# Optimization experiments

Measured on AMD Instinct MI355X. Metric: run time of the kernel, lower is better.

Reference implementation:

```python
import jax, jax.numpy as jnp
import numpy as np

N_SRC = 100_000
N_NODES = 1_000_000
N_NEIGH = 20
RAW_DIM = 256
NEIGH_DIM = 128
MSG_DIM = 128


def setup_inputs() -> dict:
    key = jax.random.key(0)
    ks = jax.random.split(key, 8)
    s = 0.05
    return {
        "raw_messages": jax.random.normal(ks[0], (N_SRC, RAW_DIM), dtype=jnp.float32),
        "neighbors": jax.random.randint(ks[1], (N_SRC, N_NEIGH), 0, N_NODES, dtype=jnp.int64),
        "memory": jax.random.normal(ks[2], (N_NODES, NEIGH_DIM), dtype=jnp.float32),
        "W1": jax.random.normal(ks[3], (RAW_DIM, RAW_DIM // 2), dtype=jnp.float32) * s,
        "b1": jnp.zeros((RAW_DIM // 2,), dtype=jnp.float32),
        "W2": jax.random.normal(ks[4], (RAW_DIM // 2, MSG_DIM), dtype=jnp.float32) * s,
        "b2": jnp.zeros((MSG_DIM,), dtype=jnp.float32),
        "Wn": jax.random.normal(ks[5], (NEIGH_DIM, MSG_DIM), dtype=jnp.float32) * s,
        "bn": jnp.zeros((MSG_DIM,), dtype=jnp.float32),
    }


def reference(raw_messages, neighbors, memory, W1, b1, W2, b2, Wn, bn):
    # Gather neighbor memories: [N, K, D_neigh]
    neighbor_memories = memory[neighbors]
    # Mean-pool over the K sampled neighbors: [N, D_neigh]
    neighbor_agg = neighbor_memories.mean(axis=1)
    # message_sum MLP: Linear -> ReLU -> Linear -> ReLU
    h = jax.nn.relu(raw_messages @ W1 + b1)
    a = jax.nn.relu(h @ W2 + b2)
    # neighbor_sum MLP: Linear -> ReLU
    b = jax.nn.relu(neighbor_agg @ Wn + bn)
    return a + b
```

## Files before the change

### kernel.cpp

```cpp
#include <hip/hip_runtime.h>

#define N_SRC    100000
#define N_NODES  1000000
#define N_NEIGH  20
#define DRAW     256
#define DH       128
#define DMSG     128
#define DNEI     128
#define LDS_PAD  8

typedef __bf16 bf16x8 __attribute__((ext_vector_type(8)));
typedef float  floatx4 __attribute__((ext_vector_type(4)));
typedef unsigned int uint32;

#define OFF_W1T   (0ull)
#define OFF_W2T   (64ull * 1024)
#define OFF_WNT   (96ull * 1024)
#define OFF_H     (1ull << 20)
#define OFF_AGG   (32ull << 20)
#define OFF_MEMBF (64ull << 20)
#define WS_NEED   (320ull << 20)

#define G1_BLOCKS   1563
#define K2_PERIODS  521
#define K2_TOTAL    (K2_PERIODS * 7)
#define CV_BLOCKS   (K2_PERIODS * 4)
#define NCHUNK      ((size_t)N_NODES * DNEI / 8)

__global__ void convert_weights(const float* __restrict__ W1,
                                const float* __restrict__ W2,
                                const float* __restrict__ Wn,
                                __bf16* __restrict__ W1t,
                                __bf16* __restrict__ W2t,
                                __bf16* __restrict__ Wnt) {
    int i = blockIdx.x * 256 + threadIdx.x;
    if (i < 32768) {
        int n = i >> 8, k = i & 255;
        W1t[i] = (__bf16)W1[k * 128 + n];
    } else if (i < 49152) {
        int j = i - 32768;
        int n = j >> 7, k = j & 127;
        W2t[j] = (__bf16)W2[k * 128 + n];
    } else {
        int j = i - 49152;
        int n = j >> 7, k = j & 127;
        Wnt[j] = (__bf16)Wn[k * 128 + n];
    }
}

__global__ __launch_bounds__(256)
void convert_and_gemm1(const float* __restrict__ raw,
                       const float* __restrict__ memv,
                       const float* __restrict__ b1,
                       const __bf16* __restrict__ W1t,
                       __bf16* __restrict__ membf,
                       __bf16* __restrict__ h) {
    __shared__ __bf16 hbuf[64][DH + LDS_PAD];

    const int bid = blockIdx.x;
    const int tid = threadIdx.x;
    const int r   = bid % 7;
    const int p   = bid / 7;

    if (r >= 3) {
        const int cvid = p * 4 + (r - 3);
        size_t c = (size_t)cvid * 256 + tid;
        const size_t stride = (size_t)CV_BLOCKS * 256;
        for (; c < NCHUNK; c += stride) {
            const floatx4* src = reinterpret_cast<const floatx4*>(memv + c * 8);
            floatx4 a = __builtin_nontemporal_load(src);
            floatx4 b = __builtin_nontemporal_load(src + 1);
            bf16x8 o;
            o[0]=(__bf16)a[0]; o[1]=(__bf16)a[1]; o[2]=(__bf16)a[2]; o[3]=(__bf16)a[3];
            o[4]=(__bf16)b[0]; o[5]=(__bf16)b[1]; o[6]=(__bf16)b[2]; o[7]=(__bf16)b[3];
            *reinterpret_cast<bf16x8*>(membf + c * 8) = o;
        }
        return;
    }

    const int g1id = p * 3 + r;
    const int s0   = g1id * 64;
    const int lane = tid & 63;
    const int wave = tid >> 6;
    const int mr   = lane & 15;
    const int quad = lane >> 4;

    {
        int rowg = s0 + wave * 16 + mr;
        int rowc = rowg < N_SRC ? rowg : N_SRC - 1;
        const float* ar = raw + (size_t)rowc * DRAW;

        floatx4 acc[8];
        #pragma unroll
        for (int nt = 0; nt < 8; ++nt) { floatx4 z = {0.f,0.f,0.f,0.f}; acc[nt] = z; }

        #pragma unroll
        for (int kk = 0; kk < DRAW; kk += 32) {
            const int kb = kk + quad * 8;
            floatx4 a0 = __builtin_nontemporal_load(
                reinterpret_cast<const floatx4*>(ar + kb));
            floatx4 a1 = __builtin_nontemporal_load(
                reinterpret_cast<const floatx4*>(ar + kb) + 1);
            bf16x8 af;
            af[0]=(__bf16)a0[0]; af[1]=(__bf16)a0[1]; af[2]=(__bf16)a0[2]; af[3]=(__bf16)a0[3];
            af[4]=(__bf16)a1[0]; af[5]=(__bf16)a1[1]; af[6]=(__bf16)a1[2]; af[7]=(__bf16)a1[3];
            #pragma unroll
            for (int nt = 0; nt < 8; ++nt) {
                bf16x8 bf = *reinterpret_cast<const bf16x8*>(
                    W1t + (nt * 16 + mr) * DRAW + kb);
                acc[nt] = __builtin_amdgcn_mfma_f32_16x16x32_bf16(af, bf, acc[nt], 0, 0, 0);
            }
        }
        #pragma unroll
        for (int nt = 0; nt < 8; ++nt) {
            const int col  = nt * 16 + mr;
            const float bias = b1[col];
            #pragma unroll
            for (int rr = 0; rr < 4; ++rr) {
                int mrow = wave * 16 + quad * 4 + rr;
                float v = acc[nt][rr] + bias;
                hbuf[mrow][col] = (__bf16)(v > 0.f ? v : 0.f);
            }
        }
    }

    __syncthreads();

    const int cr = tid >> 4;
    const int cc = (tid & 15) * 8;
    #pragma unroll
    for (int it = 0; it < 4; ++it) {
        int row = cr + it * 16;
        int rg  = s0 + row;
        if (rg < N_SRC) {
            *reinterpret_cast<bf16x8*>(h + (size_t)rg * DH + cc) =
                *reinterpret_cast<const bf16x8*>(&hbuf[row][cc]);
        }
    }
}

__global__ __launch_bounds__(256)
void gather_bf16(const int*    __restrict__ neigh,
                 const __bf16* __restrict__ membf,
                 __bf16*       __restrict__ aggb) {
    int wid0 = blockIdx.x * 4 + (threadIdx.x >> 6);
    const int wid  = __builtin_amdgcn_readfirstlane(wid0);
    const int lane = threadIdx.x & 63;
    if (wid >= N_SRC) return;

    const int* nb = neigh + wid * N_NEIGH;
    uint32 v[N_NEIGH];
    #pragma unroll
    for (int n = 0; n < N_NEIGH; ++n) {
        int idx = nb[n];
        v[n] = *reinterpret_cast<const uint32*>(
            membf + (size_t)idx * DNEI + lane * 2);
    }
    float sx = 0.f, sy = 0.f;
    #pragma unroll
    for (int n = 0; n < N_NEIGH; ++n) {
        sx += __builtin_bit_cast(float, v[n] << 16);
        sy += __builtin_bit_cast(float, v[n] & 0xffff0000u);
    }
    const float inv = 1.0f / N_NEIGH;
    __bf16 r0 = (__bf16)(sx * inv);
    __bf16 r1 = (__bf16)(sy * inv);
    union { __bf16 b[2]; uint32 u; } pk;
    pk.b[0] = r0; pk.b[1] = r1;
    *reinterpret_cast<uint32*>(aggb + (size_t)wid * DNEI + lane * 2) = pk.u;
}

__global__ __launch_bounds__(256)
void gemm23(const __bf16* __restrict__ h,
            const __bf16* __restrict__ aggb,
            const float*  __restrict__ b2,
            const float*  __restrict__ bn,
            const __bf16* __restrict__ W2t,
            const __bf16* __restrict__ Wnt,
            float* __restrict__ out) {
    const int tid  = threadIdx.x;
    const int s0   = blockIdx.x * 64;
    const int lane = tid & 63;
    const int wave = tid >> 6;
    const int mr   = lane & 15;
    const int quad = lane >> 4;

    const int rowg = s0 + wave * 16 + mr;
    const int rowc = rowg < N_SRC ? rowg : N_SRC - 1;

    bf16x8 af2[4], af3[4];
    #pragma unroll
    for (int i = 0; i < 4; ++i) {
        const int kb = i * 32 + quad * 8;
        af2[i] = *reinterpret_cast<const bf16x8*>(h    + (size_t)rowc * DH   + kb);
        af3[i] = *reinterpret_cast<const bf16x8*>(aggb + (size_t)rowc * DNEI + kb);
    }

    floatx4 acc2[8], acc3[8];
    #pragma unroll
    for (int nt = 0; nt < 8; ++nt) {
        floatx4 z = {0.f,0.f,0.f,0.f}; acc2[nt] = z; acc3[nt] = z;
    }

    #pragma unroll
    for (int i = 0; i < 4; ++i) {
        const int kb = i * 32 + quad * 8;
        #pragma unroll
        for (int nt = 0; nt < 8; ++nt) {
            bf16x8 bw2 = *reinterpret_cast<const bf16x8*>(
                W2t + (nt * 16 + mr) * DH + kb);
            acc2[nt] = __builtin_amdgcn_mfma_f32_16x16x32_bf16(af2[i], bw2, acc2[nt], 0, 0, 0);
            bf16x8 bw3 = *reinterpret_cast<const bf16x8*>(
                Wnt + (nt * 16 + mr) * DNEI + kb);
            acc3[nt] = __builtin_amdgcn_mfma_f32_16x16x32_bf16(af3[i], bw3, acc3[nt], 0, 0, 0);
        }
    }

    #pragma unroll
    for (int nt = 0; nt < 8; ++nt) {
        const int col = nt * 16 + mr;
        const float bb2 = b2[col];
        const float bbn = bn[col];
        #pragma unroll
        for (int rr = 0; rr < 4; ++rr) {
            int rowl = wave * 16 + quad * 4 + rr;
            int rg   = s0 + rowl;
            if (rg < N_SRC) {
                float va = acc2[nt][rr] + bb2; va = va > 0.f ? va : 0.f;
                float vb = acc3[nt][rr] + bbn; vb = vb > 0.f ? vb : 0.f;
                out[(size_t)rg * DMSG + col] = va + vb;
            }
        }
    }
}

__global__ __launch_bounds__(256)
void gather_mean(const int*   __restrict__ neigh,
                 const float* __restrict__ memv,
                 float*       __restrict__ agg) {
    const int wid  = blockIdx.x * 4 + (threadIdx.x >> 6);
    const int lane = threadIdx.x & 63;
    if (wid >= N_SRC) return;

    int myidx = 0;
    if (lane < N_NEIGH) myidx = neigh[wid * N_NEIGH + lane];

    float2 v[N_NEIGH];
    #pragma unroll
    for (int n = 0; n < N_NEIGH; ++n) {
        int idx = __shfl(myidx, n, 64);
        v[n] = reinterpret_cast<const float2*>(memv + (size_t)idx * DNEI)[lane];
    }
    float sx = 0.f, sy = 0.f;
    #pragma unroll
    for (int n = 0; n < N_NEIGH; ++n) { sx += v[n].x; sy += v[n].y; }
    const float inv = 1.0f / N_NEIGH;
    float2 rr; rr.x = sx * inv; rr.y = sy * inv;
    reinterpret_cast<float2*>(agg + (size_t)wid * DNEI)[lane] = rr;
}

__global__ __launch_bounds__(256)
void mlp_kernel(const float* __restrict__ raw,
                const float* __restrict__ agg,
                const float* __restrict__ b1,
                const float* __restrict__ b2,
                const float* __restrict__ bn,
                const __bf16* __restrict__ W1t,
                const __bf16* __restrict__ W2t,
                const __bf16* __restrict__ Wnt,
                float* __restrict__ out) {
    __shared__ __bf16 hbuf[64][DH + LDS_PAD];

    const int tid  = threadIdx.x;
    const int s0   = blockIdx.x * 64;
    const int lane = tid & 63;
    const int wave = tid >> 6;
    const int mr   = lane & 15;
    const int quad = lane >> 4;

    const int rowg = s0 + wave * 16 + mr;
    const int rowc = rowg < N_SRC ? rowg : N_SRC - 1;

    float4 ag[8];
    {
        const float* ar3 = agg + (size_t)rowc * DNEI;
        #pragma unroll
        for (int i = 0; i < 4; ++i) {
            ag[2 * i]     = *reinterpret_cast<const float4*>(ar3 + i * 32 + quad * 8);
            ag[2 * i + 1] = *reinterpret_cast<const float4*>(ar3 + i * 32 + quad * 8 + 4);
        }
    }

    {
        const float* ar = raw + (size_t)rowc * DRAW;
        floatx4 acc[8];
        #pragma unroll
        for (int nt = 0; nt < 8; ++nt) { floatx4 z = {0.f,0.f,0.f,0.f}; acc[nt] = z; }

        #pragma unroll
        for (int kk = 0; kk < DRAW; kk += 32) {
            const int kb = kk + quad * 8;
            float4 a0 = *reinterpret_cast<const float4*>(ar + kb);
            float4 a1 = *reinterpret_cast<const float4*>(ar + kb + 4);
            bf16x8 af;
            af[0]=(__bf16)a0.x; af[1]=(__bf16)a0.y; af[2]=(__bf16)a0.z; af[3]=(__bf16)a0.w;
            af[4]=(__bf16)a1.x; af[5]=(__bf16)a1.y; af[6]=(__bf16)a1.z; af[7]=(__bf16)a1.w;
            #pragma unroll
            for (int nt = 0; nt < 8; ++nt) {
                bf16x8 bf = *reinterpret_cast<const bf16x8*>(
                    W1t + (nt * 16 + mr) * DRAW + kb);
                acc[nt] = __builtin_amdgcn_mfma_f32_16x16x32_bf16(af, bf, acc[nt], 0, 0, 0);
            }
        }
        #pragma unroll
        for (int nt = 0; nt < 8; ++nt) {
            const int col  = nt * 16 + mr;
            const float bias = b1[col];
            #pragma unroll
            for (int rr = 0; rr < 4; ++rr) {
                int mrow = wave * 16 + quad * 4 + rr;
                float v = acc[nt][rr] + bias;
                hbuf[mrow][col] = (__bf16)(v > 0.f ? v : 0.f);
            }
        }
    }

    __syncthreads();

    {
        floatx4 acc2[8], acc3[8];
        #pragma unroll
        for (int nt = 0; nt < 8; ++nt) {
            floatx4 z = {0.f,0.f,0.f,0.f}; acc2[nt] = z; acc3[nt] = z;
        }

        #pragma unroll
        for (int kk = 0; kk < DH; kk += 32) {
            const int kb = kk + quad * 8;
            const int i  = kk >> 5;
            bf16x8 af2 = *reinterpret_cast<const bf16x8*>(&hbuf[wave * 16 + mr][kb]);
            bf16x8 af3;
            {
                float4 g0 = ag[2 * i], g1 = ag[2 * i + 1];
                af3[0]=(__bf16)g0.x; af3[1]=(__bf16)g0.y; af3[2]=(__bf16)g0.z; af3[3]=(__bf16)g0.w;
                af3[4]=(__bf16)g1.x; af3[5]=(__bf16)g1.y; af3[6]=(__bf16)g1.z; af3[7]=(__bf16)g1.w;
            }
            #pragma unroll
            for (int nt = 0; nt < 8; ++nt) {
                bf16x8 bw2 = *reinterpret_cast<const bf16x8*>(
                    W2t + (nt * 16 + mr) * DH + kb);
                acc2[nt] = __builtin_amdgcn_mfma_f32_16x16x32_bf16(af2, bw2, acc2[nt], 0, 0, 0);
                bf16x8 bw3 = *reinterpret_cast<const bf16x8*>(
                    Wnt + (nt * 16 + mr) * DNEI + kb);
                acc3[nt] = __builtin_amdgcn_mfma_f32_16x16x32_bf16(af3, bw3, acc3[nt], 0, 0, 0);
            }
        }

        #pragma unroll
        for (int nt = 0; nt < 8; ++nt) {
            const int col = nt * 16 + mr;
            const float bb2 = b2[col];
            const float bbn = bn[col];
            #pragma unroll
            for (int rr = 0; rr < 4; ++rr) {
                int rowl = wave * 16 + quad * 4 + rr;
                int rg   = s0 + rowl;
                if (rg < N_SRC) {
                    float va = acc2[nt][rr] + bb2; va = va > 0.f ? va : 0.f;
                    float vb = acc3[nt][rr] + bbn; vb = vb > 0.f ? vb : 0.f;
                    out[(size_t)rg * DMSG + col] = va + vb;
                }
            }
        }
    }
}

extern "C" void kernel_launch(void* const* d_in, const int* in_sizes, int n_in,
                              void* d_out, int out_size, void* d_ws, size_t ws_size,
                              hipStream_t stream) {
    const float* raw   = (const float*)d_in[0];
    const int*   neigh = (const int*)  d_in[1];
    const float* memv  = (const float*)d_in[2];
    const float* W1    = (const float*)d_in[3];
    const float* b1    = (const float*)d_in[4];
    const float* W2    = (const float*)d_in[5];
    const float* b2    = (const float*)d_in[6];
    const float* Wn    = (const float*)d_in[7];
    const float* bn    = (const float*)d_in[8];
    float* out = (float*)d_out;

    __bf16* W1t = (__bf16*)((char*)d_ws + OFF_W1T);
    __bf16* W2t = (__bf16*)((char*)d_ws + OFF_W2T);
    __bf16* Wnt = (__bf16*)((char*)d_ws + OFF_WNT);

    convert_weights<<<dim3(256), dim3(256), 0, stream>>>(W1, W2, Wn, W1t, W2t, Wnt);

    if (ws_size >= WS_NEED) {
        __bf16* h     = (__bf16*)((char*)d_ws + OFF_H);
        __bf16* aggb  = (__bf16*)((char*)d_ws + OFF_AGG);
        __bf16* membf = (__bf16*)((char*)d_ws + OFF_MEMBF);

        convert_and_gemm1<<<dim3(K2_TOTAL), dim3(256), 0, stream>>>(
            raw, memv, b1, W1t, membf, h);
        gather_bf16<<<dim3((N_SRC + 3) / 4), dim3(256), 0, stream>>>(
            neigh, membf, aggb);
        gemm23<<<dim3(G1_BLOCKS), dim3(256), 0, stream>>>(
            h, aggb, b2, bn, W2t, Wnt, out);
    } else {
        float* agg = out;
        gather_mean<<<dim3((N_SRC + 3) / 4), dim3(256), 0, stream>>>(neigh, memv, agg);
        mlp_kernel<<<dim3(G1_BLOCKS), dim3(256), 0, stream>>>(
            raw, agg, b1, b2, bn, W1t, W2t, Wnt, out);
    }
}
```

Before: 932.2 us.

## Split memory conversion, use 16-byte gather, fuse all three GEMMs into one kernel

Moves the fp32-to-bf16 memory conversion into its own kernel instead of interleaving it with GEMM1 blocks. The gather is rewritten so each lane loads 16 bytes and four neighbors are fetched per wave step, then reduced with cross-lane shuffles. GEMM1 is fused with GEMM2/GEMM3, keeping h in LDS so the bf16 h round-trip through global memory goes away. The cost is that the old overlap of conversion with GEMM1 is lost, and the fused kernel needs more registers.

```diff
diff --git a/kernel.cpp b/kernel.cpp
--- a/kernel.cpp
+++ b/kernel.cpp
@@ -12,20 +12,17 @@
 typedef __bf16 bf16x8 __attribute__((ext_vector_type(8)));
 typedef float  floatx4 __attribute__((ext_vector_type(4)));
 typedef unsigned int uint32;
+typedef uint32 uint32x4 __attribute__((ext_vector_type(4)));
 
 #define OFF_W1T   (0ull)
 #define OFF_W2T   (64ull * 1024)
 #define OFF_WNT   (96ull * 1024)
-#define OFF_H     (1ull << 20)
 #define OFF_AGG   (32ull << 20)
 #define OFF_MEMBF (64ull << 20)
 #define WS_NEED   (320ull << 20)
 
-#define G1_BLOCKS   1563
-#define K2_PERIODS  521
-#define K2_TOTAL    (K2_PERIODS * 7)
-#define CV_BLOCKS   (K2_PERIODS * 4)
-#define NCHUNK      ((size_t)N_NODES * DNEI / 8)
+#define G1_BLOCKS 1563
+#define NCHUNK    ((size_t)N_NODES * DNEI / 8)
 
 __global__ void convert_weights(const float* __restrict__ W1,
                                 const float* __restrict__ W2,
@@ -49,135 +46,83 @@
 }
 
 __global__ __launch_bounds__(256)
-void convert_and_gemm1(const float* __restrict__ raw,
-                       const float* __restrict__ memv,
-                       const float* __restrict__ b1,
-                       const __bf16* __restrict__ W1t,
-                       __bf16* __restrict__ membf,
-                       __bf16* __restrict__ h) {
+void convert_mem(const float* __restrict__ memv, __bf16* __restrict__ membf) {
+    size_t c = (size_t)blockIdx.x * 256 + threadIdx.x;
+    const size_t stride = (size_t)gridDim.x * 256;
+    for (; c < NCHUNK; c += stride) {
+        const floatx4* src = reinterpret_cast<const floatx4*>(memv + c * 8);
+        floatx4 a = __builtin_nontemporal_load(src);
+        floatx4 b = __builtin_nontemporal_load(src + 1);
+        bf16x8 o;
+        o[0]=(__bf16)a[0]; o[1]=(__bf16)a[1]; o[2]=(__bf16)a[2]; o[3]=(__bf16)a[3];
+        o[4]=(__bf16)b[0]; o[5]=(__bf16)b[1]; o[6]=(__bf16)b[2]; o[7]=(__bf16)b[3];
+        *reinterpret_cast<bf16x8*>(membf + c * 8) = o;
+    }
+}
+
+__global__ __launch_bounds__(256)
+void gather4(const int*    __restrict__ neigh,
+             const __bf16* __restrict__ membf,
+             __bf16*       __restrict__ aggb) {
+    const int tid   = threadIdx.x;
+    const int lane  = tid & 63;
+    const int wave  = tid >> 6;
+    const int slot  = lane >> 4;
+    const int li    = lane & 15;
+    const int sbase = blockIdx.x * 64 + wave * 16;
+
+    #pragma unroll 2
+    for (int j = 0; j < 16; ++j) {
+        const int s  = sbase + j;
+        const int sc = s < N_SRC ? s : N_SRC - 1;
+
+        int myidx = 0;
+        if (lane < N_NEIGH) myidx = neigh[sc * N_NEIGH + lane];
+
+        float acc[8];
+        #pragma unroll
+        for (int i = 0; i < 8; ++i) acc[i] = 0.f;
+
+        #pragma unroll
+        for (int n = 0; n < N_NEIGH; n += 4) {
+            int idx = __shfl(myidx, n + slot, 64);
+            uint32x4 d = *reinterpret_cast<const uint32x4*>(
+                membf + (size_t)idx * DNEI + li * 8);
+            #pragma unroll
+            for (int w = 0; w < 4; ++w) {
+                acc[2 * w]     += __builtin_bit_cast(float, d[w] << 16);
+                acc[2 * w + 1] += __builtin_bit_cast(float, d[w] & 0xffff0000u);
+            }
+        }
+
+        #pragma unroll
+        for (int i = 0; i < 8; ++i) {
+            acc[i] += __shfl_xor(acc[i], 16, 64);
+            acc[i] += __shfl_xor(acc[i], 32, 64);
+        }
+
+        if (slot == 0 && s < N_SRC) {
+            const float inv = 1.0f / N_NEIGH;
+            bf16x8 o;
+            #pragma unroll
+            for (int i = 0; i < 8; ++i) o[i] = (__bf16)(acc[i] * inv);
+            *reinterpret_cast<bf16x8*>(aggb + (size_t)s * DNEI + li * 8) = o;
+        }
+    }
+}
+
+__global__ __launch_bounds__(256)
+void mlp_kernel_b(const float*  __restrict__ raw,
+                  const __bf16* __restrict__ aggb,
+                  const float*  __restrict__ b1,
+                  const float*  __restrict__ b2,
+                  const float*  __restrict__ bn,
+                  const __bf16* __restrict__ W1t,
+                  const __bf16* __restrict__ W2t,
+                  const __bf16* __restrict__ Wnt,
+                  float* __restrict__ out) {
     __shared__ __bf16 hbuf[64][DH + LDS_PAD];
 
-    const int bid = blockIdx.x;
-    const int tid = threadIdx.x;
-    const int r   = bid % 7;
-    const int p   = bid / 7;
-
-    if (r >= 3) {
-        const int cvid = p * 4 + (r - 3);
-        size_t c = (size_t)cvid * 256 + tid;
-        const size_t stride = (size_t)CV_BLOCKS * 256;
-        for (; c < NCHUNK; c += stride) {
-            const floatx4* src = reinterpret_cast<const floatx4*>(memv + c * 8);
-            floatx4 a = __builtin_nontemporal_load(src);
-            floatx4 b = __builtin_nontemporal_load(src + 1);
-            bf16x8 o;
-            o[0]=(__bf16)a[0]; o[1]=(__bf16)a[1]; o[2]=(__bf16)a[2]; o[3]=(__bf16)a[3];
-            o[4]=(__bf16)b[0]; o[5]=(__bf16)b[1]; o[6]=(__bf16)b[2]; o[7]=(__bf16)b[3];
-            *reinterpret_cast<bf16x8*>(membf + c * 8) = o;
-        }
-        return;
-    }
-
-    const int g1id = p * 3 + r;
-    const int s0   = g1id * 64;
-    const int lane = tid & 63;
-    const int wave = tid >> 6;
-    const int mr   = lane & 15;
-    const int quad = lane >> 4;
-
-    {
-        int rowg = s0 + wave * 16 + mr;
-        int rowc = rowg < N_SRC ? rowg : N_SRC - 1;
-        const float* ar = raw + (size_t)rowc * DRAW;
-
-        floatx4 acc[8];
-        #pragma unroll
-        for (int nt = 0; nt < 8; ++nt) { floatx4 z = {0.f,0.f,0.f,0.f}; acc[nt] = z; }
-
-        #pragma unroll
-        for (int kk = 0; kk < DRAW; kk += 32) {
-            const int kb = kk + quad * 8;
-            floatx4 a0 = __builtin_nontemporal_load(
-                reinterpret_cast<const floatx4*>(ar + kb));
-            floatx4 a1 = __builtin_nontemporal_load(
-                reinterpret_cast<const floatx4*>(ar + kb) + 1);
-            bf16x8 af;
-            af[0]=(__bf16)a0[0]; af[1]=(__bf16)a0[1]; af[2]=(__bf16)a0[2]; af[3]=(__bf16)a0[3];
-            af[4]=(__bf16)a1[0]; af[5]=(__bf16)a1[1]; af[6]=(__bf16)a1[2]; af[7]=(__bf16)a1[3];
-            #pragma unroll
-            for (int nt = 0; nt < 8; ++nt) {
-                bf16x8 bf = *reinterpret_cast<const bf16x8*>(
-                    W1t + (nt * 16 + mr) * DRAW + kb);
-                acc[nt] = __builtin_amdgcn_mfma_f32_16x16x32_bf16(af, bf, acc[nt], 0, 0, 0);
-            }
-        }
-        #pragma unroll
-        for (int nt = 0; nt < 8; ++nt) {
-            const int col  = nt * 16 + mr;
-            const float bias = b1[col];
-            #pragma unroll
-            for (int rr = 0; rr < 4; ++rr) {
-                int mrow = wave * 16 + quad * 4 + rr;
-                float v = acc[nt][rr] + bias;
-                hbuf[mrow][col] = (__bf16)(v > 0.f ? v : 0.f);
-            }
-        }
-    }
-
-    __syncthreads();
-
-    const int cr = tid >> 4;
-    const int cc = (tid & 15) * 8;
-    #pragma unroll
-    for (int it = 0; it < 4; ++it) {
-        int row = cr + it * 16;
-        int rg  = s0 + row;
-        if (rg < N_SRC) {
-            *reinterpret_cast<bf16x8*>(h + (size_t)rg * DH + cc) =
-                *reinterpret_cast<const bf16x8*>(&hbuf[row][cc]);
-        }
-    }
-}
-
-__global__ __launch_bounds__(256)
-void gather_bf16(const int*    __restrict__ neigh,
-                 const __bf16* __restrict__ membf,
-                 __bf16*       __restrict__ aggb) {
-    int wid0 = blockIdx.x * 4 + (threadIdx.x >> 6);
-    const int wid  = __builtin_amdgcn_readfirstlane(wid0);
-    const int lane = threadIdx.x & 63;
-    if (wid >= N_SRC) return;
-
-    const int* nb = neigh + wid * N_NEIGH;
-    uint32 v[N_NEIGH];
-    #pragma unroll
-    for (int n = 0; n < N_NEIGH; ++n) {
-        int idx = nb[n];
-        v[n] = *reinterpret_cast<const uint32*>(
-            membf + (size_t)idx * DNEI + lane * 2);
-    }
-    float sx = 0.f, sy = 0.f;
-    #pragma unroll
-    for (int n = 0; n < N_NEIGH; ++n) {
-        sx += __builtin_bit_cast(float, v[n] << 16);
-        sy += __builtin_bit_cast(float, v[n] & 0xffff0000u);
-    }
-    const float inv = 1.0f / N_NEIGH;
-    __bf16 r0 = (__bf16)(sx * inv);
-    __bf16 r1 = (__bf16)(sy * inv);
-    union { __bf16 b[2]; uint32 u; } pk;
-    pk.b[0] = r0; pk.b[1] = r1;
-    *reinterpret_cast<uint32*>(aggb + (size_t)wid * DNEI + lane * 2) = pk.u;
-}
-
-__global__ __launch_bounds__(256)
-void gemm23(const __bf16* __restrict__ h,
-            const __bf16* __restrict__ aggb,
-            const float*  __restrict__ b2,
-            const float*  __restrict__ bn,
-            const __bf16* __restrict__ W2t,
-            const __bf16* __restrict__ Wnt,
-            float* __restrict__ out) {
     const int tid  = threadIdx.x;
     const int s0   = blockIdx.x * 64;
     const int lane = tid & 63;
@@ -188,47 +133,87 @@
     const int rowg = s0 + wave * 16 + mr;
     const int rowc = rowg < N_SRC ? rowg : N_SRC - 1;
 
-    bf16x8 af2[4], af3[4];
-    #pragma unroll
-    for (int i = 0; i < 4; ++i) {
-        const int kb = i * 32 + quad * 8;
-        af2[i] = *reinterpret_cast<const bf16x8*>(h    + (size_t)rowc * DH   + kb);
-        af3[i] = *reinterpret_cast<const bf16x8*>(aggb + (size_t)rowc * DNEI + kb);
-    }
-
-    floatx4 acc2[8], acc3[8];
-    #pragma unroll
-    for (int nt = 0; nt < 8; ++nt) {
-        floatx4 z = {0.f,0.f,0.f,0.f}; acc2[nt] = z; acc3[nt] = z;
-    }
-
-    #pragma unroll
-    for (int i = 0; i < 4; ++i) {
-        const int kb = i * 32 + quad * 8;
-        #pragma unroll
-        for (int nt = 0; nt < 8; ++nt) {
-            bf16x8 bw2 = *reinterpret_cast<const bf16x8*>(
-                W2t + (nt * 16 + mr) * DH + kb);
-            acc2[nt] = __builtin_amdgcn_mfma_f32_16x16x32_bf16(af2[i], bw2, acc2[nt], 0, 0, 0);
-            bf16x8 bw3 = *reinterpret_cast<const bf16x8*>(
-                Wnt + (nt * 16 + mr) * DNEI + kb);
-            acc3[nt] = __builtin_amdgcn_mfma_f32_16x16x32_bf16(af3[i], bw3, acc3[nt], 0, 0, 0);
-        }
-    }
-
-    #pragma unroll
-    for (int nt = 0; nt < 8; ++nt) {
-        const int col = nt * 16 + mr;
-        const float bb2 = b2[col];
-        const float bbn = bn[col];
-        #pragma unroll
-        for (int rr = 0; rr < 4; ++rr) {
-            int rowl = wave * 16 + quad * 4 + rr;
-            int rg   = s0 + rowl;
-            if (rg < N_SRC) {
-                float va = acc2[nt][rr] + bb2; va = va > 0.f ? va : 0.f;
-                float vb = acc3[nt][rr] + bbn; vb = vb > 0.f ? vb : 0.f;
-                out[(size_t)rg * DMSG + col] = va + vb;
+    bf16x8 af3[4];
+    {
+        const __bf16* ar3 = aggb + (size_t)rowc * DNEI;
+        #pragma unroll
+        for (int i = 0; i < 4; ++i)
+            af3[i] = *reinterpret_cast<const bf16x8*>(ar3 + i * 32 + quad * 8);
+    }
+
+    {
+        const float* ar = raw + (size_t)rowc * DRAW;
+        floatx4 acc[8];
+        #pragma unroll
+        for (int nt = 0; nt < 8; ++nt) { floatx4 z = {0.f,0.f,0.f,0.f}; acc[nt] = z; }
+
+        #pragma unroll
+        for (int kk = 0; kk < DRAW; kk += 32) {
+            const int kb = kk + quad * 8;
+            float4 a0 = *reinterpret_cast<const float4*>(ar + kb);
+            float4 a1 = *reinterpret_cast<const float4*>(ar + kb + 4);
+            bf16x8 af;
+            af[0]=(__bf16)a0.x; af[1]=(__bf16)a0.y; af[2]=(__bf16)a0.z; af[3]=(__bf16)a0.w;
+            af[4]=(__bf16)a1.x; af[5]=(__bf16)a1.y; af[6]=(__bf16)a1.z; af[7]=(__bf16)a1.w;
+            #pragma unroll
+            for (int nt = 0; nt < 8; ++nt) {
+                bf16x8 bf = *reinterpret_cast<const bf16x8*>(
+                    W1t + (nt * 16 + mr) * DRAW + kb);
+                acc[nt] = __builtin_amdgcn_mfma_f32_16x16x32_bf16(af, bf, acc[nt], 0, 0, 0);
+            }
+        }
+        #pragma unroll
+        for (int nt = 0; nt < 8; ++nt) {
+            const int col  = nt * 16 + mr;
+            const float bias = b1[col];
+            #pragma unroll
+            for (int rr = 0; rr < 4; ++rr) {
+                int mrow = wave * 16 + quad * 4 + rr;
+                float v = acc[nt][rr] + bias;
+                hbuf[mrow][col] = (__bf16)(v > 0.f ? v : 0.f);
+            }
+        }
+    }
+
+    __syncthreads();
+
+    {
+        floatx4 acc2[8], acc3[8];
+        #pragma unroll
+        for (int nt = 0; nt < 8; ++nt) {
+            floatx4 z = {0.f,0.f,0.f,0.f}; acc2[nt] = z; acc3[nt] = z;
+        }
+
+        #pragma unroll
+        for (int kk = 0; kk < DH; kk += 32) {
+            const int kb = kk + quad * 8;
+            const int i  = kk >> 5;
+            bf16x8 af2 = *reinterpret_cast<const bf16x8*>(&hbuf[wave * 16 + mr][kb]);
+            #pragma unroll
+            for (int nt = 0; nt < 8; ++nt) {
+                bf16x8 bw2 = *reinterpret_cast<const bf16x8*>(
+                    W2t + (nt * 16 + mr) * DH + kb);
+                acc2[nt] = __builtin_amdgcn_mfma_f32_16x16x32_bf16(af2, bw2, acc2[nt], 0, 0, 0);
+                bf16x8 bw3 = *reinterpret_cast<const bf16x8*>(
+                    Wnt + (nt * 16 + mr) * DNEI + kb);
+                acc3[nt] = __builtin_amdgcn_mfma_f32_16x16x32_bf16(af3[i], bw3, acc3[nt], 0, 0, 0);
+            }
+        }
+
+        #pragma unroll
+        for (int nt = 0; nt < 8; ++nt) {
+            const int col = nt * 16 + mr;
+            const float bb2 = b2[col];
+            const float bbn = bn[col];
+            #pragma unroll
+            for (int rr = 0; rr < 4; ++rr) {
+                int rowl = wave * 16 + quad * 4 + rr;
+                int rg   = s0 + rowl;
+                if (rg < N_SRC) {
+                    float va = acc2[nt][rr] + bb2; va = va > 0.f ? va : 0.f;
+                    float vb = acc3[nt][rr] + bbn; vb = vb > 0.f ? vb : 0.f;
+                    out[(size_t)rg * DMSG + col] = va + vb;
+                }
             }
         }
     }
@@ -396,16 +381,13 @@
     convert_weights<<<dim3(256), dim3(256), 0, stream>>>(W1, W2, Wn, W1t, W2t, Wnt);
 
     if (ws_size >= WS_NEED) {
-        __bf16* h     = (__bf16*)((char*)d_ws + OFF_H);
         __bf16* aggb  = (__bf16*)((char*)d_ws + OFF_AGG);
         __bf16* membf = (__bf16*)((char*)d_ws + OFF_MEMBF);
 
-        convert_and_gemm1<<<dim3(K2_TOTAL), dim3(256), 0, stream>>>(
-            raw, memv, b1, W1t, membf, h);
-        gather_bf16<<<dim3((N_SRC + 3) / 4), dim3(256), 0, stream>>>(
-            neigh, membf, aggb);
-        gemm23<<<dim3(G1_BLOCKS), dim3(256), 0, stream>>>(
-            h, aggb, b2, bn, W2t, Wnt, out);
+        convert_mem<<<dim3(2048), dim3(256), 0, stream>>>(memv, membf);
+        gather4<<<dim3(G1_BLOCKS), dim3(256), 0, stream>>>(neigh, membf, aggb);
+        mlp_kernel_b<<<dim3(G1_BLOCKS), dim3(256), 0, stream>>>(
+            raw, aggb, b1, b2, bn, W1t, W2t, Wnt, out);
     } else {
         float* agg = out;
         gather_mean<<<dim3((N_SRC + 3) / 4), dim3(256), 0, stream>>>(neigh, memv, agg);
```

After: 949.3 us. About the same (+1.8%).
